# Performance work log

Measured on AMD Instinct MI355X. Metric: run time of the kernel, lower is better.

## Reference

```python
import jax, jax.numpy as jnp
import numpy as np

B, N, H, D = 4, 2048, 8, 64
DM = 512  # model dim = H * D


def setup_inputs() -> dict:
    key = jax.random.key(0)
    ks = jax.random.split(key, 8)
    x = jax.random.normal(ks[0], (B, N, DM), dtype=jnp.float32)
    mask_k = jax.random.randint(ks[1], (B, N), 0, 5) > 0
    mask_q = jax.random.randint(ks[2], (B, N), 0, 5) > 0
    s_in = 1.0 / np.sqrt(DM)
    s_out = 1.0 / np.sqrt(H * D)
    Wq = jax.random.normal(ks[3], (DM, H * D), dtype=jnp.float32) * s_in
    Wk = jax.random.normal(ks[4], (DM, H * D), dtype=jnp.float32) * s_in
    Wv = jax.random.normal(ks[5], (DM, H * D), dtype=jnp.float32) * s_in
    Wo = jax.random.normal(ks[6], (H * D, DM), dtype=jnp.float32) * s_out
    bo = jnp.zeros((DM,), dtype=jnp.float32)
    return {"x": x, "Wq": Wq, "Wk": Wk, "Wv": Wv, "Wo": Wo, "bo": bo,
            "mask_k": mask_k, "mask_q": mask_q}


def reference(x, Wq, Wk, Wv, Wo, bo, mask_k, mask_q):
    b, n, _ = x.shape
    # projections (no bias), split into heads: b n (h d) -> b n h d
    q = (x @ Wq).reshape(b, n, H, D)
    k = (x @ Wk).reshape(b, n, H, D)
    v = (x @ Wv).reshape(b, n, H, D)
    scale = D ** (-0.5)
    sim = jnp.einsum('bihd,bjhd->bijh', q, k) * scale  # [b, i, j, h]
    big_neg = jnp.finfo(jnp.float32).min
    sim = jnp.where(mask_k[:, None, :, None], sim, big_neg)
    sim = jnp.where(mask_q[:, :, None, None], sim, big_neg)
    attn = jax.nn.softmax(sim, axis=-2)  # softmax over key axis j
    out = jnp.einsum('bijh,bjhd->bihd', attn, v).reshape(b, n, H * D)
    return out @ Wo + bo
```

## Files before the change

### kernel.cpp

```cpp
#include <hip/hip_runtime.h>

typedef _Float16 f16;
typedef _Float16 f16x8 __attribute__((ext_vector_type(8)));
typedef float    f32x4 __attribute__((ext_vector_type(4)));

#define MFMA16(A, B, C) __builtin_amdgcn_mfma_f32_16x16x32_f16((A), (B), (C), 0, 0, 0)

__device__ __forceinline__ void gl_lds16(const void* g, void* l) {
  __builtin_amdgcn_global_load_lds(
      (const __attribute__((address_space(1))) void*)g,
      (__attribute__((address_space(3))) void*)l, 16, 0, 0);
}

static constexpr size_t OFF_XH  = 0;
static constexpr size_t OFF_WQT = 8388608;
static constexpr size_t OFF_WOT = OFF_WQT + 3 * 524288;
static constexpr size_t OFF_QH  = OFF_WOT + 524288;
static constexpr size_t OFF_KH  = OFF_QH + 8388608;
static constexpr size_t OFF_VT  = OFF_KH + 8388608;
static constexpr size_t OFF_A2  = OFF_VT + 8388608;

#define QSCALE 0.18033688011112042f
#define NEGFIX -11.541560327111708f

__global__ void k_cvt_x(const float* __restrict__ x, f16* __restrict__ xh) {
  int i = blockIdx.x * blockDim.x + threadIdx.x;
  const float4* p = (const float4*)x + (size_t)i * 2;
  float4 a = p[0], b = p[1];
  f16x8 o = { (f16)a.x, (f16)a.y, (f16)a.z, (f16)a.w,
              (f16)b.x, (f16)b.y, (f16)b.z, (f16)b.w };
  *((f16x8*)xh + i) = o;
}

__global__ void k_cvt_w4(const float* __restrict__ w0, const float* __restrict__ w1,
                         const float* __restrict__ w2, const float* __restrict__ w3,
                         f16* __restrict__ dst) {
  __shared__ float tile[32][33];
  const int z = blockIdx.z;
  const float* w = (z == 0) ? w0 : (z == 1) ? w1 : (z == 2) ? w2 : w3;
  const float sc = (z == 0) ? QSCALE : 1.0f;
  f16* wt = dst + (size_t)z * 262144;
  int tx = threadIdx.x & 31, ty = threadIdx.x >> 5;
  int bx = blockIdx.x, by = blockIdx.y;
#pragma unroll
  for (int i = 0; i < 32; i += 8)
    tile[ty + i][tx] = w[(size_t)(by * 32 + ty + i) * 512 + bx * 32 + tx];
  __syncthreads();
#pragma unroll
  for (int i = 0; i < 32; i += 8)
    wt[(size_t)(bx * 32 + ty + i) * 512 + by * 32 + tx] = (f16)(tile[tx][ty + i] * sc);
}

template <int MODE, int BN>
__global__ __launch_bounds__(256, 2)
void k_gemm(const f16* __restrict__ A, const f16* __restrict__ Bt,
            void* __restrict__ O0, void* __restrict__ O1, void* __restrict__ O2,
            const float* __restrict__ bias) {
  constexpr int NF = BN / 32;
  constexpr int PB = BN / 32;
  constexpr int ABYTES = 16384;
  constexpr int BBYTES = BN * 128;
  constexpr int SM_STAGE  = 2 * (ABYTES + BBYTES);
  constexpr int SM_BOUNCE = (MODE == 3) ? 128 * 136 * 2 : 0;
  constexpr int SM = SM_STAGE > SM_BOUNCE ? SM_STAGE : SM_BOUNCE;
  __shared__ __align__(16) char smem[SM];
  const int t = threadIdx.x;
  const int lane = t & 63, w = t >> 6;
  const int wr = w >> 1, wc = w & 1;
  const int l15 = lane & 15, l4 = lane >> 4;
  const int lr = lane >> 3, lc = lane & 7;
  const int row0 = blockIdx.y * 128;
  const int col0 = blockIdx.x * BN;

  f32x4 acc[4][NF] = {};

  auto stage = [&](int kt, int buf) {
    char* dA = smem + buf * ABYTES + w * 1024;
    char* dB = smem + 2 * ABYTES + buf * BBYTES + w * 1024;
#pragma unroll
    for (int p = 0; p < 4; ++p) {
      int r = p * 32 + w * 8 + lr;
      gl_lds16((const char*)A + ((size_t)(row0 + r) * 512 + kt) * 2 + ((lc ^ (r & 7)) << 4),
               dA + p * 4096);
    }
#pragma unroll
    for (int p = 0; p < PB; ++p) {
      int r = p * 32 + w * 8 + lr;
      gl_lds16((const char*)Bt + ((size_t)(col0 + r) * 512 + kt) * 2 + ((lc ^ (r & 7)) << 4),
               dB + p * 4096);
    }
  };

  stage(0, 0);
  for (int ks = 0; ks < 8; ++ks) {
    const int buf = ks & 1;
    __syncthreads();
    if (ks < 7) stage((ks + 1) * 64, buf ^ 1);
    const char* cA = smem + buf * ABYTES;
    const char* cB = smem + 2 * ABYTES + buf * BBYTES;
    __builtin_amdgcn_s_setprio(1);
#pragma unroll
    for (int kb = 0; kb < 2; ++kb) {
      f16x8 af[4], bf[NF];
#pragma unroll
      for (int m = 0; m < 4; ++m) {
        int r = wr * 64 + m * 16 + l15;
        int lb = r * 128 + kb * 64 + l4 * 16;
        af[m] = *(const f16x8*)(cA + (lb ^ ((r & 7) << 4)));
      }
#pragma unroll
      for (int n = 0; n < NF; ++n) {
        int r = wc * (BN / 2) + n * 16 + l15;
        int lb = r * 128 + kb * 64 + l4 * 16;
        bf[n] = *(const f16x8*)(cB + (lb ^ ((r & 7) << 4)));
      }
#pragma unroll
      for (int m = 0; m < 4; ++m)
#pragma unroll
        for (int n = 0; n < NF; ++n)
          acc[m][n] = MFMA16(af[m], bf[n], acc[m][n]);
    }
    __builtin_amdgcn_s_setprio(0);
  }

  if (MODE == 2) {
#pragma unroll
    for (int m = 0; m < 4; ++m)
#pragma unroll
      for (int n = 0; n < NF; ++n) {
        int gr = row0 + wr * 64 + m * 16 + l4 * 4;
        int gc = col0 + wc * (BN / 2) + n * 16 + l15;
        float* C = (float*)O0;
        float bv = bias[gc];
#pragma unroll
        for (int rr = 0; rr < 4; ++rr)
          C[(size_t)(gr + rr) * 512 + gc] = acc[m][n][rr] + bv;
      }
  } else {
    int seg = col0 >> 9;
    if (seg < 2) {
      __syncthreads();
      f16* bb = (f16*)smem;
#pragma unroll
      for (int m = 0; m < 4; ++m)
#pragma unroll
        for (int n = 0; n < NF; ++n) {
          int r = wr * 64 + m * 16 + l4 * 4;
          int c = wc * (BN / 2) + n * 16 + l15;
#pragma unroll
          for (int rr = 0; rr < 4; ++rr)
            bb[(r + rr) * 136 + c] = (f16)acc[m][n][rr];
        }
      __syncthreads();
      f16* C = (f16*)(seg == 0 ? O0 : O1);
      int cbase = col0 & 511;
#pragma unroll
      for (int i = 0; i < 8; ++i) {
        int idx = i * 256 + t;
        int r = idx >> 4, c8 = (idx & 15) * 8;
        uint4 v = *(const uint4*)(bb + r * 136 + c8);
        *(uint4*)(C + (size_t)(row0 + r) * 512 + cbase + c8) = v;
      }
    } else {
#pragma unroll
      for (int m = 0; m < 4; ++m)
#pragma unroll
        for (int n = 0; n < NF; ++n) {
          int gr = row0 + wr * 64 + m * 16 + l4 * 4;
          int lcol = (col0 & 511) + wc * (BN / 2) + n * 16 + l15;
          f16* C = (f16*)O2;
          int hh = lcol >> 6, dd = lcol & 63;
          int bb2 = gr >> 11, ns = gr & 2047;
          union { uint2 u2; f16 v[4]; } pk;
#pragma unroll
          for (int rr = 0; rr < 4; ++rr) pk.v[rr] = (f16)acc[m][n][rr];
          *(uint2*)(C + (size_t)((bb2 * 8 + hh) * 64 + dd) * 2048 + ns) = pk.u2;
        }
    }
  }
}

__global__ __launch_bounds__(256, 3)
void k_attn(const f16* __restrict__ Q, const f16* __restrict__ K,
            const f16* __restrict__ Vt, const int* __restrict__ mask_k,
            const int* __restrict__ mask_q, f16* __restrict__ A2) {
  __shared__ __align__(16) f16 sK[2][64 * 64];
  __shared__ __align__(16) f16 sV[2][64 * 64];
  __shared__ __align__(16) f16 sP[4][32 * 64];
  const int t = threadIdx.x, lane = t & 63, w = t >> 6;
  const int l15 = lane & 15, l4 = lane >> 4;
  const int lr = lane >> 3, lc = lane & 7;
  const int bh = blockIdx.y, b = bh >> 3, h = bh & 7;
  const int q0 = blockIdx.x * 128 + w * 32;

  f16x8 qa[2][2];
  int mqi[2][4];
#pragma unroll
  for (int g = 0; g < 2; ++g) {
    const f16* qb = Q + (size_t)(b * 2048 + q0 + g * 16 + l15) * 512 + h * 64 + l4 * 8;
    qa[g][0] = *(const f16x8*)qb;
    qa[g][1] = *(const f16x8*)(qb + 32);
#pragma unroll
    for (int rr = 0; rr < 4; ++rr)
      mqi[g][rr] = mask_q[b * 2048 + q0 + g * 16 + l4 * 4 + rr];
  }

  const f16x8 onesv = { (f16)1.f, (f16)1.f, (f16)1.f, (f16)1.f,
                        (f16)1.f, (f16)1.f, (f16)1.f, (f16)1.f };
  f32x4 o[2][4] = {};
  f32x4 oex[2] = {};

  const char* Kbase  = (const char*)K + ((size_t)b * 2048 * 512 + h * 64) * 2;
  const char* VtBase = (const char*)Vt + ((size_t)(b * 8 + h) * 64) * 2048 * 2;
  char* sPw = (char*)&sP[w][0];

  auto stage = [&](int kv, int buf) {
#pragma unroll
    for (int p = 0; p < 2; ++p) {
      int r = p * 32 + w * 8 + lr;
      gl_lds16(Kbase + (size_t)(kv + r) * 1024 + ((lc ^ (r & 7)) << 4),
               (char*)&sK[buf][0] + p * 4096 + w * 1024);
      gl_lds16(VtBase + ((size_t)r * 2048 + kv) * 2 + ((lc ^ (r & 7)) << 4),
               (char*)&sV[buf][0] + p * 4096 + w * 1024);
    }
  };

  stage(0, 0);
  for (int it = 0; it < 32; ++it) {
    const int kv = it * 64, buf = it & 1;
    __syncthreads();
    if (it < 31) stage(kv + 64, buf ^ 1);

    int mk[4];
#pragma unroll
    for (int jf = 0; jf < 4; ++jf)
      mk[jf] = mask_k[b * 2048 + kv + jf * 16 + l15];

    f32x4 s[2][4];
    __builtin_amdgcn_s_setprio(1);
#pragma unroll
    for (int jf = 0; jf < 4; ++jf) {
      int r = jf * 16 + l15;
      int base = r * 128 + l4 * 16;
      f16x8 b0 = *(const f16x8*)((const char*)&sK[buf][0] + (base ^ ((r & 7) << 4)));
      f16x8 b1 = *(const f16x8*)((const char*)&sK[buf][0] + ((base + 64) ^ ((r & 7) << 4)));
#pragma unroll
      for (int g = 0; g < 2; ++g) {
        f32x4 z = { NEGFIX, NEGFIX, NEGFIX, NEGFIX };
        z = MFMA16(qa[g][0], b0, z);
        z = MFMA16(qa[g][1], b1, z);
        s[g][jf] = z;
      }
    }
    __builtin_amdgcn_s_setprio(0);

#pragma unroll
    for (int g = 0; g < 2; ++g)
#pragma unroll
      for (int jf = 0; jf < 4; ++jf)
#pragma unroll
        for (int rr = 0; rr < 4; ++rr) {
          float sv = s[g][jf][rr];
          sv = mk[jf] ? sv : -1000.0f;
          sv = mqi[g][rr] ? sv : -8.0f;
          float p = __builtin_amdgcn_exp2f(sv);
          int row = g * 16 + l4 * 4 + rr;
          int boff = row * 128 + (jf * 16 + l15) * 2;
          *(f16*)(sPw + (boff ^ ((row & 7) << 4))) = (f16)p;
        }

    __builtin_amdgcn_s_setprio(1);
#pragma unroll
    for (int kb = 0; kb < 2; ++kb) {
      f16x8 pa[2];
#pragma unroll
      for (int g = 0; g < 2; ++g) {
        int r = g * 16 + l15;
        int base = r * 128 + kb * 64 + l4 * 16;
        pa[g] = *(const f16x8*)(sPw + (base ^ ((r & 7) << 4)));
        oex[g] = MFMA16(pa[g], onesv, oex[g]);
      }
#pragma unroll
      for (int df = 0; df < 4; ++df) {
        int r = df * 16 + l15;
        int base = r * 128 + kb * 64 + l4 * 16;
        f16x8 bv = *(const f16x8*)((const char*)&sV[buf][0] + (base ^ ((r & 7) << 4)));
#pragma unroll
        for (int g = 0; g < 2; ++g)
          o[g][df] = MFMA16(pa[g], bv, o[g][df]);
      }
    }
    __builtin_amdgcn_s_setprio(0);
  }

#pragma unroll
  for (int g = 0; g < 2; ++g) {
    float inv[4];
#pragma unroll
    for (int rr = 0; rr < 4; ++rr) inv[rr] = 1.0f / oex[g][rr];
#pragma unroll
    for (int df = 0; df < 4; ++df)
#pragma unroll
      for (int rr = 0; rr < 4; ++rr)
        A2[(size_t)(b * 2048 + q0 + g * 16 + l4 * 4 + rr) * 512 + h * 64 + df * 16 + l15] =
            (f16)(o[g][df][rr] * inv[rr]);
  }
}

extern "C" void kernel_launch(void* const* d_in, const int* in_sizes, int n_in,
                              void* d_out, int out_size, void* d_ws, size_t ws_size,
                              hipStream_t stream) {
  (void)in_sizes; (void)n_in; (void)out_size; (void)ws_size;
  const float* x   = (const float*)d_in[0];
  const float* Wq  = (const float*)d_in[1];
  const float* Wk  = (const float*)d_in[2];
  const float* Wv  = (const float*)d_in[3];
  const float* Wo  = (const float*)d_in[4];
  const float* bo  = (const float*)d_in[5];
  const int* mask_k = (const int*)d_in[6];
  const int* mask_q = (const int*)d_in[7];
  float* out = (float*)d_out;
  char* ws = (char*)d_ws;

  f16* Xh   = (f16*)(ws + OFF_XH);
  f16* Wqkv = (f16*)(ws + OFF_WQT);
  f16* Wot  = (f16*)(ws + OFF_WOT);
  f16* Qh   = (f16*)(ws + OFF_QH);
  f16* Kh   = (f16*)(ws + OFF_KH);
  f16* Vt   = (f16*)(ws + OFF_VT);
  f16* A2   = (f16*)(ws + OFF_A2);

  k_cvt_x<<<2048, 256, 0, stream>>>(x, Xh);
  k_cvt_w4<<<dim3(16, 16, 4), 256, 0, stream>>>(Wq, Wk, Wv, Wo, Wqkv);

  k_gemm<3, 128><<<dim3(12, 64), 256, 0, stream>>>(Xh, Wqkv, Qh, Kh, Vt, nullptr);

  k_attn<<<dim3(16, 32), 256, 0, stream>>>(Qh, Kh, Vt, mask_k, mask_q, A2);

  k_gemm<2, 128><<<dim3(4, 64), 256, 0, stream>>>(A2, Wot, out, nullptr, nullptr, bo);
}
```

Before: 173.5 us.

## Enlarge attention KV tile, transpose score MFMA, precompute key-mask bias, swizzle grids

```diff
diff --git a/kernel.cpp b/kernel.cpp
--- a/kernel.cpp
+++ b/kernel.cpp
@@ -1,6 +1,7 @@
 #include <hip/hip_runtime.h>
 
 typedef _Float16 f16;
+typedef __fp16   fp16x2 __attribute__((ext_vector_type(2)));
 typedef _Float16 f16x8 __attribute__((ext_vector_type(8)));
 typedef float    f32x4 __attribute__((ext_vector_type(4)));
 
@@ -19,17 +20,20 @@
 static constexpr size_t OFF_KH  = OFF_QH + 8388608;
 static constexpr size_t OFF_VT  = OFF_KH + 8388608;
 static constexpr size_t OFF_A2  = OFF_VT + 8388608;
+static constexpr size_t OFF_AMK = OFF_A2 + 8388608;
 
 #define QSCALE 0.18033688011112042f
 #define NEGFIX -11.541560327111708f
 
-__global__ void k_cvt_x(const float* __restrict__ x, f16* __restrict__ xh) {
+__global__ void k_cvt_x(const float* __restrict__ x, f16* __restrict__ xh,
+                        const int* __restrict__ mask_k, float* __restrict__ amk) {
   int i = blockIdx.x * blockDim.x + threadIdx.x;
   const float4* p = (const float4*)x + (size_t)i * 2;
   float4 a = p[0], b = p[1];
   f16x8 o = { (f16)a.x, (f16)a.y, (f16)a.z, (f16)a.w,
               (f16)b.x, (f16)b.y, (f16)b.z, (f16)b.w };
   *((f16x8*)xh + i) = o;
+  if (i < 8192) amk[i] = mask_k[i] ? 0.0f : -1000.0f;
 }
 
 __global__ void k_cvt_w4(const float* __restrict__ w0, const float* __restrict__ w1,
@@ -51,14 +55,14 @@
     wt[(size_t)(bx * 32 + ty + i) * 512 + by * 32 + tx] = (f16)(tile[tx][ty + i] * sc);
 }
 
-template <int MODE, int BN>
-__global__ __launch_bounds__(256, 2)
+template <int MODE, int BM, int BN>
+__global__ __launch_bounds__(256, (MODE == 2 ? 3 : 2))
 void k_gemm(const f16* __restrict__ A, const f16* __restrict__ Bt,
             void* __restrict__ O0, void* __restrict__ O1, void* __restrict__ O2,
             const float* __restrict__ bias) {
-  constexpr int NF = BN / 32;
-  constexpr int PB = BN / 32;
-  constexpr int ABYTES = 16384;
+  constexpr int MR = BM / 32, NF = BN / 32;
+  constexpr int AP = BM / 32, BP = BN / 32;
+  constexpr int ABYTES = BM * 128;
   constexpr int BBYTES = BN * 128;
   constexpr int SM_STAGE  = 2 * (ABYTES + BBYTES);
   constexpr int SM_BOUNCE = (MODE == 3) ? 128 * 136 * 2 : 0;
@@ -69,22 +73,25 @@
   const int wr = w >> 1, wc = w & 1;
   const int l15 = lane & 15, l4 = lane >> 4;
   const int lr = lane >> 3, lc = lane & 7;
-  const int row0 = blockIdx.y * 128;
-  const int col0 = blockIdx.x * BN;
-
-  f32x4 acc[4][NF] = {};
+  const int flat = blockIdx.x + gridDim.x * blockIdx.y;
+  const int nwg  = gridDim.x * gridDim.y;
+  const int sw   = (flat & 7) * (nwg >> 3) + (flat >> 3);
+  const int row0 = (sw / gridDim.x) * BM;
+  const int col0 = (sw % gridDim.x) * BN;
+
+  f32x4 acc[MR][NF] = {};
 
   auto stage = [&](int kt, int buf) {
     char* dA = smem + buf * ABYTES + w * 1024;
     char* dB = smem + 2 * ABYTES + buf * BBYTES + w * 1024;
 #pragma unroll
-    for (int p = 0; p < 4; ++p) {
+    for (int p = 0; p < AP; ++p) {
       int r = p * 32 + w * 8 + lr;
       gl_lds16((const char*)A + ((size_t)(row0 + r) * 512 + kt) * 2 + ((lc ^ (r & 7)) << 4),
                dA + p * 4096);
     }
 #pragma unroll
-    for (int p = 0; p < PB; ++p) {
+    for (int p = 0; p < BP; ++p) {
       int r = p * 32 + w * 8 + lr;
       gl_lds16((const char*)Bt + ((size_t)(col0 + r) * 512 + kt) * 2 + ((lc ^ (r & 7)) << 4),
                dB + p * 4096);
@@ -101,10 +108,10 @@
     __builtin_amdgcn_s_setprio(1);
 #pragma unroll
     for (int kb = 0; kb < 2; ++kb) {
-      f16x8 af[4], bf[NF];
-#pragma unroll
-      for (int m = 0; m < 4; ++m) {
-        int r = wr * 64 + m * 16 + l15;
+      f16x8 af[MR], bf[NF];
+#pragma unroll
+      for (int m = 0; m < MR; ++m) {
+        int r = wr * (BM / 2) + m * 16 + l15;
         int lb = r * 128 + kb * 64 + l4 * 16;
         af[m] = *(const f16x8*)(cA + (lb ^ ((r & 7) << 4)));
       }
@@ -115,7 +122,7 @@
         bf[n] = *(const f16x8*)(cB + (lb ^ ((r & 7) << 4)));
       }
 #pragma unroll
-      for (int m = 0; m < 4; ++m)
+      for (int m = 0; m < MR; ++m)
 #pragma unroll
         for (int n = 0; n < NF; ++n)
           acc[m][n] = MFMA16(af[m], bf[n], acc[m][n]);
@@ -125,10 +132,10 @@
 
   if (MODE == 2) {
 #pragma unroll
-    for (int m = 0; m < 4; ++m)
+    for (int m = 0; m < MR; ++m)
 #pragma unroll
       for (int n = 0; n < NF; ++n) {
-        int gr = row0 + wr * 64 + m * 16 + l4 * 4;
+        int gr = row0 + wr * (BM / 2) + m * 16 + l4 * 4;
         int gc = col0 + wc * (BN / 2) + n * 16 + l15;
         float* C = (float*)O0;
         float bv = bias[gc];
@@ -142,10 +149,10 @@
       __syncthreads();
       f16* bb = (f16*)smem;
 #pragma unroll
-      for (int m = 0; m < 4; ++m)
+      for (int m = 0; m < MR; ++m)
 #pragma unroll
         for (int n = 0; n < NF; ++n) {
-          int r = wr * 64 + m * 16 + l4 * 4;
+          int r = wr * (BM / 2) + m * 16 + l4 * 4;
           int c = wc * (BN / 2) + n * 16 + l15;
 #pragma unroll
           for (int rr = 0; rr < 4; ++rr)
@@ -163,10 +170,10 @@
       }
     } else {
 #pragma unroll
-      for (int m = 0; m < 4; ++m)
+      for (int m = 0; m < MR; ++m)
 #pragma unroll
         for (int n = 0; n < NF; ++n) {
-          int gr = row0 + wr * 64 + m * 16 + l4 * 4;
+          int gr = row0 + wr * (BM / 2) + m * 16 + l4 * 4;
           int lcol = (col0 & 511) + wc * (BN / 2) + n * 16 + l15;
           f16* C = (f16*)O2;
           int hh = lcol >> 6, dd = lcol & 63;
@@ -180,29 +187,31 @@
   }
 }
 
-__global__ __launch_bounds__(256, 3)
+__global__ __launch_bounds__(256, 2)
 void k_attn(const f16* __restrict__ Q, const f16* __restrict__ K,
-            const f16* __restrict__ Vt, const int* __restrict__ mask_k,
+            const f16* __restrict__ Vt, const float* __restrict__ amk,
             const int* __restrict__ mask_q, f16* __restrict__ A2) {
-  __shared__ __align__(16) f16 sK[2][64 * 64];
-  __shared__ __align__(16) f16 sV[2][64 * 64];
+  __shared__ __align__(16) f16 sK[2][128 * 64];
+  __shared__ __align__(16) f16 sV[2][64 * 128];
   __shared__ __align__(16) f16 sP[4][32 * 64];
   const int t = threadIdx.x, lane = t & 63, w = t >> 6;
   const int l15 = lane & 15, l4 = lane >> 4;
   const int lr = lane >> 3, lc = lane & 7;
-  const int bh = blockIdx.y, b = bh >> 3, h = bh & 7;
-  const int q0 = blockIdx.x * 128 + w * 32;
+  const int sw = (blockIdx.x & 7) * 64 + (blockIdx.x >> 3);
+  const int qx = sw & 15, bh = sw >> 4;
+  const int b = bh >> 3, h = bh & 7;
+  const int q0 = qx * 128 + w * 32;
 
   f16x8 qa[2][2];
-  int mqi[2][4];
+  float qm[2], qo[2];
 #pragma unroll
   for (int g = 0; g < 2; ++g) {
     const f16* qb = Q + (size_t)(b * 2048 + q0 + g * 16 + l15) * 512 + h * 64 + l4 * 8;
     qa[g][0] = *(const f16x8*)qb;
     qa[g][1] = *(const f16x8*)(qb + 32);
-#pragma unroll
-    for (int rr = 0; rr < 4; ++rr)
-      mqi[g][rr] = mask_q[b * 2048 + q0 + g * 16 + l4 * 4 + rr];
+    int mq = mask_q[b * 2048 + q0 + g * 16 + l15];
+    qm[g] = mq ? 1.0f : 0.0f;
+    qo[g] = mq ? 0.0f : -8.0f;
   }
 
   const f16x8 onesv = { (f16)1.f, (f16)1.f, (f16)1.f, (f16)1.f,
@@ -212,85 +221,105 @@
 
   const char* Kbase  = (const char*)K + ((size_t)b * 2048 * 512 + h * 64) * 2;
   const char* VtBase = (const char*)Vt + ((size_t)(b * 8 + h) * 64) * 2048 * 2;
+  const float* amkb = amk + b * 2048;
   char* sPw = (char*)&sP[w][0];
 
   auto stage = [&](int kv, int buf) {
 #pragma unroll
-    for (int p = 0; p < 2; ++p) {
+    for (int p = 0; p < 4; ++p) {
       int r = p * 32 + w * 8 + lr;
       gl_lds16(Kbase + (size_t)(kv + r) * 1024 + ((lc ^ (r & 7)) << 4),
                (char*)&sK[buf][0] + p * 4096 + w * 1024);
-      gl_lds16(VtBase + ((size_t)r * 2048 + kv) * 2 + ((lc ^ (r & 7)) << 4),
+    }
+#pragma unroll
+    for (int p = 0; p < 4; ++p) {
+      int d = p * 16 + w * 4 + (lane >> 4);
+      int c = lane & 15;
+      gl_lds16(VtBase + ((size_t)d * 2048 + kv) * 2 + ((c ^ (d & 7)) << 4),
                (char*)&sV[buf][0] + p * 4096 + w * 1024);
     }
   };
 
   stage(0, 0);
-  for (int it = 0; it < 32; ++it) {
-    const int kv = it * 64, buf = it & 1;
+  for (int it = 0; it < 16; ++it) {
+    const int kv = it * 128, buf = it & 1;
     __syncthreads();
-    if (it < 31) stage(kv + 64, buf ^ 1);
-
-    int mk[4];
-#pragma unroll
-    for (int jf = 0; jf < 4; ++jf)
-      mk[jf] = mask_k[b * 2048 + kv + jf * 16 + l15];
-
-    f32x4 s[2][4];
-    __builtin_amdgcn_s_setprio(1);
-#pragma unroll
-    for (int jf = 0; jf < 4; ++jf) {
-      int r = jf * 16 + l15;
-      int base = r * 128 + l4 * 16;
-      f16x8 b0 = *(const f16x8*)((const char*)&sK[buf][0] + (base ^ ((r & 7) << 4)));
-      f16x8 b1 = *(const f16x8*)((const char*)&sK[buf][0] + ((base + 64) ^ ((r & 7) << 4)));
-#pragma unroll
-      for (int g = 0; g < 2; ++g) {
-        f32x4 z = { NEGFIX, NEGFIX, NEGFIX, NEGFIX };
-        z = MFMA16(qa[g][0], b0, z);
-        z = MFMA16(qa[g][1], b1, z);
-        s[g][jf] = z;
-      }
-    }
-    __builtin_amdgcn_s_setprio(0);
-
-#pragma unroll
-    for (int g = 0; g < 2; ++g)
+    if (it < 15) stage(kv + 128, buf ^ 1);
+    const char* cK = (const char*)&sK[buf][0];
+    const char* cV = (const char*)&sV[buf][0];
+
+#pragma unroll
+    for (int h2 = 0; h2 < 2; ++h2) {
+      f32x4 sT[2][4];
+      __builtin_amdgcn_s_setprio(1);
+#pragma unroll
+      for (int jf = 0; jf < 4; ++jf) {
+        int r = h2 * 64 + jf * 16 + l15;
+        int base = r * 128 + l4 * 16;
+        f16x8 k0 = *(const f16x8*)(cK + (base ^ ((r & 7) << 4)));
+        f16x8 k1 = *(const f16x8*)(cK + ((base + 64) ^ ((r & 7) << 4)));
+#pragma unroll
+        for (int g = 0; g < 2; ++g) {
+          f32x4 z = { NEGFIX, NEGFIX, NEGFIX, NEGFIX };
+          z = MFMA16(k0, qa[g][0], z);
+          z = MFMA16(k1, qa[g][1], z);
+          sT[g][jf] = z;
+        }
+      }
+      __builtin_amdgcn_s_setprio(0);
+
+      f32x4 amv[4];
 #pragma unroll
       for (int jf = 0; jf < 4; ++jf)
-#pragma unroll
-        for (int rr = 0; rr < 4; ++rr) {
-          float sv = s[g][jf][rr];
-          sv = mk[jf] ? sv : -1000.0f;
-          sv = mqi[g][rr] ? sv : -8.0f;
-          float p = __builtin_amdgcn_exp2f(sv);
-          int row = g * 16 + l4 * 4 + rr;
-          int boff = row * 128 + (jf * 16 + l15) * 2;
-          *(f16*)(sPw + (boff ^ ((row & 7) << 4))) = (f16)p;
-        }
-
-    __builtin_amdgcn_s_setprio(1);
-#pragma unroll
-    for (int kb = 0; kb < 2; ++kb) {
-      f16x8 pa[2];
-#pragma unroll
-      for (int g = 0; g < 2; ++g) {
-        int r = g * 16 + l15;
-        int base = r * 128 + kb * 64 + l4 * 16;
-        pa[g] = *(const f16x8*)(sPw + (base ^ ((r & 7) << 4)));
-        oex[g] = MFMA16(pa[g], onesv, oex[g]);
-      }
-#pragma unroll
-      for (int df = 0; df < 4; ++df) {
-        int r = df * 16 + l15;
-        int base = r * 128 + kb * 64 + l4 * 16;
-        f16x8 bv = *(const f16x8*)((const char*)&sV[buf][0] + (base ^ ((r & 7) << 4)));
-#pragma unroll
-        for (int g = 0; g < 2; ++g)
-          o[g][df] = MFMA16(pa[g], bv, o[g][df]);
-      }
-    }
-    __builtin_amdgcn_s_setprio(0);
+        amv[jf] = *(const f32x4*)(amkb + kv + h2 * 64 + jf * 16 + l4 * 4);
+#pragma unroll
+      for (int g = 0; g < 2; ++g)
+#pragma unroll
+        for (int jf = 0; jf < 4; ++jf) {
+          float p0 = __builtin_amdgcn_exp2f(
+              __builtin_fmaf(amv[jf][0], qm[g],
+                  __builtin_fmaf(sT[g][jf][0], qm[g], qo[g])));
+          float p1 = __builtin_amdgcn_exp2f(
+              __builtin_fmaf(amv[jf][1], qm[g],
+                  __builtin_fmaf(sT[g][jf][1], qm[g], qo[g])));
+          float p2 = __builtin_amdgcn_exp2f(
+              __builtin_fmaf(amv[jf][2], qm[g],
+                  __builtin_fmaf(sT[g][jf][2], qm[g], qo[g])));
+          float p3 = __builtin_amdgcn_exp2f(
+              __builtin_fmaf(amv[jf][3], qm[g],
+                  __builtin_fmaf(sT[g][jf][3], qm[g], qo[g])));
+          fp16x2 a01 = __builtin_amdgcn_cvt_pkrtz(p0, p1);
+          fp16x2 a23 = __builtin_amdgcn_cvt_pkrtz(p2, p3);
+          uint2 pk = { __builtin_bit_cast(unsigned, a01),
+                       __builtin_bit_cast(unsigned, a23) };
+          int row = g * 16 + l15;
+          int boff = row * 128 + jf * 32 + l4 * 8;
+          *(uint2*)(sPw + (boff ^ ((row & 7) << 4))) = pk;
+        }
+
+      __builtin_amdgcn_s_setprio(1);
+#pragma unroll
+      for (int kb = 0; kb < 2; ++kb) {
+        f16x8 pa[2];
+#pragma unroll
+        for (int g = 0; g < 2; ++g) {
+          int rq = g * 16 + l15;
+          int pbase = rq * 128 + kb * 64 + l4 * 16;
+          pa[g] = *(const f16x8*)(sPw + (pbase ^ ((rq & 7) << 4)));
+          oex[g] = MFMA16(pa[g], onesv, oex[g]);
+        }
+#pragma unroll
+        for (int df = 0; df < 4; ++df) {
+          int d = df * 16 + l15;
+          int vbase = d * 256 + h2 * 128 + kb * 64 + l4 * 16;
+          f16x8 bv = *(const f16x8*)(cV + (vbase ^ ((d & 7) << 4)));
+#pragma unroll
+          for (int g = 0; g < 2; ++g)
+            o[g][df] = MFMA16(pa[g], bv, o[g][df]);
+        }
+      }
+      __builtin_amdgcn_s_setprio(0);
+    }
   }
 
 #pragma unroll
@@ -329,13 +358,14 @@
   f16* Kh   = (f16*)(ws + OFF_KH);
   f16* Vt   = (f16*)(ws + OFF_VT);
   f16* A2   = (f16*)(ws + OFF_A2);
-
-  k_cvt_x<<<2048, 256, 0, stream>>>(x, Xh);
+  float* AMK = (float*)(ws + OFF_AMK);
+
+  k_cvt_x<<<2048, 256, 0, stream>>>(x, Xh, mask_k, AMK);
   k_cvt_w4<<<dim3(16, 16, 4), 256, 0, stream>>>(Wq, Wk, Wv, Wo, Wqkv);
 
-  k_gemm<3, 128><<<dim3(12, 64), 256, 0, stream>>>(Xh, Wqkv, Qh, Kh, Vt, nullptr);
-
-  k_attn<<<dim3(16, 32), 256, 0, stream>>>(Qh, Kh, Vt, mask_k, mask_q, A2);
-
-  k_gemm<2, 128><<<dim3(4, 64), 256, 0, stream>>>(A2, Wot, out, nullptr, nullptr, bo);
-}
+  k_gemm<3, 128, 128><<<dim3(12, 64), 256, 0, stream>>>(Xh, Wqkv, Qh, Kh, Vt, nullptr);
+
+  k_attn<<<512, 256, 0, stream>>>(Qh, Kh, Vt, AMK, mask_q, A2);
+
+  k_gemm<2, 128, 64><<<dim3(8, 64), 256, 0, stream>>>(A2, Wot, out, nullptr, nullptr, bo);
+}
```

Result: faster. 158.7 us (-8.5%).
